# Optimization experiments

Hardware: AMD Instinct MI355X
Metric: run time of the kernel (lower is better)

Reference implementation:

```python
import jax, jax.numpy as jnp
import numpy as np

B, L, EMB, H, NL, E, MAXA, PAD = 64, 512, 400, 256, 3, 512, 32, 0


def setup_inputs() -> dict:
    key = jax.random.key(0)
    ks = jax.random.split(key, 12)
    s = lambda k, shape: jax.random.normal(k, shape, jnp.float32) * 0.02
    Semb = jax.random.normal(ks[0], (B, EMB, L), jnp.float32)
    word_ids = jax.random.randint(ks[1], (B, L), 0, 30000)
    y1 = jax.random.randint(ks[2], (B,), 0, L - MAXA)
    span = jax.random.randint(ks[3], (B,), 0, MAXA)
    y2 = y1 + span
    edges = jax.random.randint(ks[4], (B, E, 2), 0, L)
    return dict(
        Semb=Semb,
        ans_sent_word_ids=word_ids,
        y1_in_sent=y1,
        y2_in_sent=y2,
        edges=edges,
        W1=s(ks[5], (H, EMB)),                 # Initialized_Conv1d (k=1, no bias)
        hw_lin_W=s(ks[6], (2, H, H)), hw_lin_b=jnp.zeros((2, H), jnp.float32),
        hw_gate_W=s(ks[7], (2, H, H)), hw_gate_b=jnp.zeros((2, H), jnp.float32),
        gcn_W=s(ks[8], (NL, H, H)), gcn_b=jnp.zeros((NL, H), jnp.float32),
        conv_W=s(ks[9], (1, NL * H)), conv_b=jnp.zeros((1,), jnp.float32),
        lin_W=s(ks[10], (L, L)), lin_b=jnp.zeros((L,), jnp.float32),
    )


def reference(Semb, ans_sent_word_ids, y1_in_sent, y2_in_sent, edges,
              W1, hw_lin_W, hw_lin_b, hw_gate_W, hw_gate_b,
              gcn_W, gcn_b, conv_W, conv_b, lin_W, lin_b):
    # 1x1 conv: [B, EMB, L] -> [B, H, L]
    x = jnp.einsum('oi,bit->bot', W1, Semb)
    # 2-layer Highway (dropout is identity in eval)
    for i in range(2):
        gate = jax.nn.sigmoid(jnp.einsum('oi,bit->bot', hw_gate_W[i], x) + hw_gate_b[i][None, :, None])
        nonlin = jnp.einsum('oi,bit->bot', hw_lin_W[i], x) + hw_lin_b[i][None, :, None]
        x = gate * nonlin + (1.0 - gate) * x
    maskS = (ans_sent_word_ids != PAD).astype(x.dtype)            # [B, L]
    # answer-span mask (Aemb itself is dead code in the original forward's output)
    pos = y1_in_sent[:, None] + jnp.arange(MAXA)                   # [B, MAXA]
    maskA = (pos <= y2_in_sent[:, None]).astype(x.dtype)
    # dense adjacency from edge list (undirected since gcn_directed=False)
    bidx = jnp.broadcast_to(jnp.arange(B)[:, None], (B, E))
    adj = jnp.zeros((B, L, L), x.dtype)
    adj = adj.at[bidx, edges[..., 0], edges[..., 1]].set(1.0)
    adj = adj.at[bidx, edges[..., 1], edges[..., 0]].set(1.0)
    # GCN (C-GCN style: W(Ax) + W(x), note bias counted twice, /(deg+1), relu)
    h = x.transpose(0, 2, 1)                                       # [B, L, H]
    denom = jnp.sum(adj, axis=2, keepdims=True) + 1.0              # [B, L, 1]
    outs = []
    for l in range(NL):
        Ax = jnp.einsum('bls,bsh->blh', adj, h)
        AxW = jnp.einsum('blh,oh->blo', Ax + h, gcn_W[l]) + 2.0 * gcn_b[l]
        h = jax.nn.relu(AxW / denom)
        outs.append(h)
    cat = jnp.concatenate(outs, axis=2)                            # [B, L, NL*H]
    y = jax.nn.relu(jnp.einsum('blc,oc->bol', cat, conv_W) + conv_b[None, :, None])  # [B,1,L]
    logits = (jnp.einsum('bol,ml->bom', y, lin_W) + lin_b).squeeze(1)                # [B,L]
    logits = logits * maskS + (1.0 - maskS) * (-1e30)
    return (logits, maskA)
```

## Files before the change

### kernel.cpp

```cpp
#include <hip/hip_runtime.h>
#include <cstdint>

#define B 64
#define L 512
#define EMB 400
#define KPAD 416
#define H 256
#define NL 3
#define NE 512
#define MAXA 32
#define M_TOT (B * L)

typedef unsigned short u16;
typedef float f32x4 __attribute__((ext_vector_type(4)));
typedef short short8 __attribute__((ext_vector_type(8)));
typedef u16 u16x8 __attribute__((ext_vector_type(8)));

__device__ __forceinline__ float b2f(u16 u) {
  unsigned v = ((unsigned)u) << 16;
  return __builtin_bit_cast(float, v);
}
__device__ __forceinline__ u16 f2b(float f) {
  unsigned u = __builtin_bit_cast(unsigned, f);
  unsigned r = (u + 0x7fffu + ((u >> 16) & 1u)) >> 16;
  return (u16)r;
}

#define GL16(g, l)                                                              \
  __builtin_amdgcn_global_load_lds((const __attribute__((address_space(1))) void*)(g), \
                                   (__attribute__((address_space(3))) void*)(l), 16, 0, 0)

__global__ __launch_bounds__(256, 2) void k_convT(const float* __restrict__ Semb,
                                                  const u16* __restrict__ W1b,
                                                  u16* __restrict__ Out) {
  __shared__ u16 smem[64 * KPAD + 256 * 32];
  u16* At = smem;
  u16* Bt = smem + 64 * KPAD;
  u16 (*tmp)[72] = (u16(*)[72])Bt;

  const int t = threadIdx.x;
  const int wid = t >> 6, lane = t & 63;
  const int m0 = blockIdx.x * 64;
  const int b = m0 >> 9, l0 = m0 & 511;
  const int fr = lane & 15, kg = lane >> 4;
  const int r4 = t >> 2, ksg = t & 3;

  for (int et = 0; et < 7; ++et) {
    const int e0 = et * 64;
    const int erows = (et < 6) ? 64 : 32;
    {
      const int er = t >> 2, ls = (t & 3) * 16;
      if (er < erows) {
        if (e0 + er < EMB) {
          const float* src = Semb + ((size_t)b * EMB + e0 + er) * L + l0 + ls;
#pragma unroll
          for (int i = 0; i < 4; ++i) {
            const float4 v = *(const float4*)(src + i * 4);
            tmp[er][ls + i * 4 + 0] = f2b(v.x);
            tmp[er][ls + i * 4 + 1] = f2b(v.y);
            tmp[er][ls + i * 4 + 2] = f2b(v.z);
            tmp[er][ls + i * 4 + 3] = f2b(v.w);
          }
        } else {
#pragma unroll
          for (int i = 0; i < 16; ++i) tmp[er][ls + i] = 0;
        }
      }
    }
    __syncthreads();
    {
      const int lr = t >> 2, es = (t & 3) * 16;
      if (es < erows) {
        u16x8 v0, v1;
#pragma unroll
        for (int i = 0; i < 8; ++i) v0[i] = tmp[es + i][lr];
#pragma unroll
        for (int i = 0; i < 8; ++i) v1[i] = tmp[es + 8 + i][lr];
        const int k = e0 + es;
        u16* dst = At + (((size_t)(k >> 5) * 64 + lr) * 4 + ((k & 31) >> 3)) * 8;
        *(u16x8*)dst = v0;
        *(u16x8*)(dst + 8) = v1;
      }
    }
    __syncthreads();
  }

  f32x4 acc[4][4] = {};
  for (int kk = 0; kk < (KPAD >> 5); ++kk) {
    const int kc = kk * 32 + ksg * 8;
#pragma unroll
    for (int c = 0; c < 4; ++c)
      GL16(W1b + (size_t)(c * 64 + r4) * KPAD + kc, Bt + (size_t)(c * 256 + wid * 64) * 8);
    asm volatile("s_waitcnt vmcnt(0)" ::: "memory");
    __builtin_amdgcn_s_barrier();
    asm volatile("" ::: "memory");
    short8 af[4], bf[4];
#pragma unroll
    for (int i = 0; i < 4; ++i) {
      af[i] = *(const short8*)(At + ((size_t)(kk * 64 + i * 16 + fr) * 4 + kg) * 8);
      bf[i] = *(const short8*)(Bt + ((size_t)(wid * 64 + i * 16 + fr) * 4 + kg) * 8);
    }
#pragma unroll
    for (int mi = 0; mi < 4; ++mi)
#pragma unroll
      for (int ni = 0; ni < 4; ++ni)
        acc[mi][ni] = __builtin_amdgcn_mfma_f32_16x16x32_bf16(af[mi], bf[ni], acc[mi][ni], 0, 0, 0);
    __builtin_amdgcn_s_barrier();
    asm volatile("" ::: "memory");
  }

  const int r0 = kg * 4;
  const int c0 = wid * 64 + fr;
#pragma unroll
  for (int ni = 0; ni < 4; ++ni) {
    const int col = c0 + ni * 16;
#pragma unroll
    for (int mi = 0; mi < 4; ++mi)
#pragma unroll
      for (int rr = 0; rr < 4; ++rr)
        Out[(size_t)(m0 + mi * 16 + r0 + rr) * H + col] = f2b(acc[mi][ni][rr]);
  }
}

__global__ __launch_bounds__(256, 2) void gemm64hw(
    const u16* __restrict__ A, const u16* __restrict__ Bw, const u16* __restrict__ B2w,
    const float* __restrict__ bias1, const float* __restrict__ bias2,
    u16* __restrict__ Out) {
  __shared__ u16 Bl[2 * 256 * 32];
  __shared__ u16 Cl[2 * 256 * 32];
  __shared__ u16 Al[2 * 64 * 32];

  const int t = threadIdx.x;
  const int wid = t >> 6, lane = t & 63;
  const int m0 = blockIdx.x * 64;
  const int fr = lane & 15, kg = lane >> 4;
  const int r4 = t >> 2, ksg = t & 3;

  f32x4 acc[4][4] = {};
  f32x4 acc2[4][4] = {};

  for (int kk = 0; kk < 4; ++kk) {
#pragma unroll
    for (int h = 0; h < 2; ++h) {
      const int kc = kk * 64 + h * 32 + ksg * 8;
#pragma unroll
      for (int c = 0; c < 4; ++c) {
        GL16(Bw + (size_t)(c * 64 + r4) * H + kc,
             Bl + (size_t)h * 8192 + (size_t)(c * 256 + wid * 64) * 8);
        GL16(B2w + (size_t)(c * 64 + r4) * H + kc,
             Cl + (size_t)h * 8192 + (size_t)(c * 256 + wid * 64) * 8);
      }
      GL16(A + (size_t)(m0 + r4) * H + kc,
           Al + (size_t)h * 2048 + (size_t)(wid * 64) * 8);
    }
    asm volatile("s_waitcnt vmcnt(0)" ::: "memory");
    __builtin_amdgcn_s_barrier();
    asm volatile("" ::: "memory");
#pragma unroll
    for (int h = 0; h < 2; ++h) {
      short8 af[4], bf[4], cf[4];
#pragma unroll
      for (int i = 0; i < 4; ++i) {
        af[i] = *(const short8*)(Al + (size_t)h * 2048 + ((size_t)(i * 16 + fr) * 4 + kg) * 8);
        bf[i] = *(const short8*)(Bl + (size_t)h * 8192 +
                                 ((size_t)(wid * 64 + i * 16 + fr) * 4 + kg) * 8);
        cf[i] = *(const short8*)(Cl + (size_t)h * 8192 +
                                 ((size_t)(wid * 64 + i * 16 + fr) * 4 + kg) * 8);
      }
#pragma unroll
      for (int mi = 0; mi < 4; ++mi)
#pragma unroll
        for (int ni = 0; ni < 4; ++ni) {
          acc[mi][ni] =
              __builtin_amdgcn_mfma_f32_16x16x32_bf16(af[mi], bf[ni], acc[mi][ni], 0, 0, 0);
          acc2[mi][ni] =
              __builtin_amdgcn_mfma_f32_16x16x32_bf16(af[mi], cf[ni], acc2[mi][ni], 0, 0, 0);
        }
    }
    __builtin_amdgcn_s_barrier();
    asm volatile("" ::: "memory");
  }

  const int r0 = kg * 4;
  const int c0 = wid * 64 + fr;
#pragma unroll
  for (int ni = 0; ni < 4; ++ni) {
    const int col = c0 + ni * 16;
    const float b1 = bias1[col], b2 = bias2[col];
#pragma unroll
    for (int mi = 0; mi < 4; ++mi)
#pragma unroll
      for (int rr = 0; rr < 4; ++rr) {
        const int row = m0 + mi * 16 + r0 + rr;
        const float g = 1.f / (1.f + __expf(-(acc[mi][ni][rr] + b1)));
        const float nn = acc2[mi][ni][rr] + b2;
        const float x = b2f(A[(size_t)row * H + col]);
        Out[(size_t)row * H + col] = f2b(g * nn + (1.f - g) * x);
      }
  }
}

template <bool LAST>
__global__ __launch_bounds__(256, 2) void gemm64gcn(
    const u16* __restrict__ A, const u16* __restrict__ Bw,
    const float* __restrict__ bias1, const float* __restrict__ rden,
    const float* __restrict__ cw, float* __restrict__ yv, u16* __restrict__ Out) {
  __shared__ u16 Bl0[2 * 256 * 32];
  __shared__ u16 Bl1[2 * 256 * 32];
  __shared__ u16 Al0[2 * 64 * 32];
  __shared__ u16 Al1[2 * 64 * 32];

  const int t = threadIdx.x;
  const int wid = t >> 6, lane = t & 63;
  const int m0 = blockIdx.x * 64;
  const int fr = lane & 15, kg = lane >> 4;
  const int r4 = t >> 2, ksg = t & 3;

  f32x4 acc[4][4] = {};

  auto stage = [&](u16* Ab, u16* Bb, int kk) {
#pragma unroll
    for (int h = 0; h < 2; ++h) {
      const int kc = kk * 64 + h * 32 + ksg * 8;
#pragma unroll
      for (int c = 0; c < 4; ++c)
        GL16(Bw + (size_t)(c * 64 + r4) * H + kc,
             Bb + (size_t)h * 8192 + (size_t)(c * 256 + wid * 64) * 8);
      GL16(A + (size_t)(m0 + r4) * H + kc,
           Ab + (size_t)h * 2048 + (size_t)(wid * 64) * 8);
    }
  };
  auto compute = [&](const u16* Ab, const u16* Bb) {
#pragma unroll
    for (int h = 0; h < 2; ++h) {
      short8 af[4], bf[4];
#pragma unroll
      for (int i = 0; i < 4; ++i) {
        af[i] = *(const short8*)(Ab + (size_t)h * 2048 + ((size_t)(i * 16 + fr) * 4 + kg) * 8);
        bf[i] = *(const short8*)(Bb + (size_t)h * 8192 +
                                 ((size_t)(wid * 64 + i * 16 + fr) * 4 + kg) * 8);
      }
#pragma unroll
      for (int mi = 0; mi < 4; ++mi)
#pragma unroll
        for (int ni = 0; ni < 4; ++ni)
          acc[mi][ni] =
              __builtin_amdgcn_mfma_f32_16x16x32_bf16(af[mi], bf[ni], acc[mi][ni], 0, 0, 0);
    }
  };

  const int nk = H >> 6;
  stage(Al0, Bl0, 0);
  for (int kk = 0; kk < nk; ++kk) {
    u16* Ac = (kk & 1) ? Al1 : Al0;
    u16* Bc = (kk & 1) ? Bl1 : Bl0;
    u16* An = (kk & 1) ? Al0 : Al1;
    u16* Bn = (kk & 1) ? Bl0 : Bl1;
    if (kk + 1 < nk) {
      stage(An, Bn, kk + 1);
      asm volatile("s_waitcnt vmcnt(10)" ::: "memory");
    } else {
      asm volatile("s_waitcnt vmcnt(0)" ::: "memory");
    }
    __builtin_amdgcn_s_barrier();
    asm volatile("" ::: "memory");
    compute(Ac, Bc);
    __builtin_amdgcn_s_barrier();
    asm volatile("" ::: "memory");
  }

  const int r0 = kg * 4;
  const int c0 = wid * 64 + fr;
  float ypart[16];
#pragma unroll
  for (int q = 0; q < 16; ++q) ypart[q] = 0.f;
#pragma unroll
  for (int ni = 0; ni < 4; ++ni) {
    const int col = c0 + ni * 16;
    const float b1 = 2.f * bias1[col];
    const float cwv = cw[col];
#pragma unroll
    for (int mi = 0; mi < 4; ++mi)
#pragma unroll
      for (int rr = 0; rr < 4; ++rr) {
        const int row = m0 + mi * 16 + r0 + rr;
        const float s = (acc[mi][ni][rr] + b1) * rden[row];
        const float rl = s > 0.f ? s : 0.f;
        ypart[mi * 4 + rr] += rl * cwv;
        if constexpr (!LAST) Out[(size_t)row * H + col] = f2b(rl);
      }
  }
#pragma unroll
  for (int q = 0; q < 16; ++q) {
    float p = ypart[q];
    p += __shfl_xor(p, 1);
    p += __shfl_xor(p, 2);
    p += __shfl_xor(p, 4);
    p += __shfl_xor(p, 8);
    if (fr == 0) atomicAdd(&yv[m0 + (q >> 2) * 16 + r0 + (q & 3)], p);
  }
}

__global__ __launch_bounds__(256) void k_gather(const unsigned* __restrict__ bm,
                                                const u16* __restrict__ h,
                                                u16* __restrict__ T) {
  const int t = threadIdx.x;
  const int tok = blockIdx.x * 8 + (t >> 5);
  const int b = tok >> 9;
  const int c = (t & 31) * 8;
  const uint4* wp4 = (const uint4*)(bm + (size_t)tok * 16);
  const uint4 w0 = wp4[0], w1 = wp4[1], w2 = wp4[2], w3 = wp4[3];
  const unsigned wa[16] = {w0.x, w0.y, w0.z, w0.w, w1.x, w1.y, w1.z, w1.w,
                           w2.x, w2.y, w2.z, w2.w, w3.x, w3.y, w3.z, w3.w};
  float acc[8];
  {
    const u16x8 v = *(const u16x8*)(h + (size_t)tok * H + c);
#pragma unroll
    for (int i = 0; i < 8; ++i) acc[i] = b2f(v[i]);
  }
#pragma unroll
  for (int wi = 0; wi < 16; ++wi) {
    unsigned bits = wa[wi];
    while (bits) {
      const int bit = __ffs(bits) - 1;
      bits &= bits - 1;
      const int s = wi * 32 + bit;
      const u16x8 u = *(const u16x8*)(h + (size_t)(b * L + s) * H + c);
#pragma unroll
      for (int i = 0; i < 8; ++i) acc[i] += b2f(u[i]);
    }
  }
  u16x8 o;
#pragma unroll
  for (int i = 0; i < 8; ++i) o[i] = f2b(acc[i]);
  *(u16x8*)(T + (size_t)tok * H + c) = o;
}

__global__ __launch_bounds__(256) void k_prep2(const int* __restrict__ edges,
                                               unsigned* __restrict__ bm,
                                               float* __restrict__ rden,
                                               float* __restrict__ yv,
                                               const float* __restrict__ W1,
                                               const float* __restrict__ gW,
                                               const float* __restrict__ lW,
                                               const float* __restrict__ gcnW,
                                               u16* __restrict__ W1b, u16* __restrict__ HWGb,
                                               u16* __restrict__ HWLb, u16* __restrict__ GCNb) {
  const int t = threadIdx.x;
  if (blockIdx.x < B) {
    __shared__ unsigned lbm[512 * 16];
    const int b = blockIdx.x;
#pragma unroll
    for (int i = 0; i < 32; ++i) lbm[i * 256 + t] = 0;
    __syncthreads();
#pragma unroll
    for (int e = 0; e < 2; ++e) {
      const int idx = t * 2 + e;
      const int u = edges[((size_t)b * NE + idx) * 2 + 0];
      const int v = edges[((size_t)b * NE + idx) * 2 + 1];
      atomicOr(&lbm[u * 16 + (v >> 5)], 1u << (v & 31));
      atomicOr(&lbm[v * 16 + (u >> 5)], 1u << (u & 31));
    }
    __syncthreads();
    uint4* gbm = (uint4*)(bm + (size_t)b * 512 * 16);
    const uint4* lb4 = (const uint4*)lbm;
#pragma unroll
    for (int i = 0; i < 8; ++i) gbm[i * 256 + t] = lb4[i * 256 + t];
#pragma unroll
    for (int r = 0; r < 2; ++r) {
      const int row = t * 2 + r;
      int c = 0;
#pragma unroll
      for (int w = 0; w < 16; ++w) c += __popc(lbm[row * 16 + w]);
      rden[(size_t)b * 512 + row] = 1.f / (1.f + (float)c);
    }
#pragma unroll
    for (int i = 0; i < 2; ++i) yv[(size_t)b * 512 + i * 256 + t] = 0.f;
    return;
  }
  int i = (blockIdx.x - B) * 256 + t;
  if (i < 256 * KPAD) {
    const int o = i / KPAD, k = i - o * KPAD;
    W1b[i] = (k < EMB) ? f2b(W1[o * EMB + k]) : (u16)0;
    return;
  }
  i -= 256 * KPAD;
  if (i < 2 * H * H) { HWGb[i] = f2b(gW[i]); return; }
  i -= 2 * H * H;
  if (i < 2 * H * H) { HWLb[i] = f2b(lW[i]); return; }
  i -= 2 * H * H;
  if (i < NL * H * H) GCNb[i] = f2b(gcnW[i]);
}

__global__ __launch_bounds__(256) void k_logits(const float* __restrict__ yv,
                                                const float* __restrict__ cb,
                                                const float* __restrict__ lw,
                                                const float* __restrict__ lb,
                                                const int* __restrict__ wids,
                                                const int* __restrict__ y1,
                                                const int* __restrict__ y2,
                                                float* __restrict__ out) {
  if (blockIdx.x == B * 2) {
#pragma unroll
    for (int j = 0; j < 8; ++j) {
      const int idx = j * 256 + threadIdx.x;
      const int b = idx >> 5, q = idx & 31;
      out[B * L + idx] = (y1[b] + q <= y2[b]) ? 1.0f : 0.0f;
    }
    return;
  }
  const int b = blockIdx.x >> 1;
  const int m = ((blockIdx.x & 1) << 8) + threadIdx.x;
  __shared__ float ys[512];
  const float cb0 = cb[0];
  ys[threadIdx.x] = fmaxf(yv[(size_t)b * L + threadIdx.x] + cb0, 0.f);
  ys[threadIdx.x + 256] = fmaxf(yv[(size_t)b * L + 256 + threadIdx.x] + cb0, 0.f);
  __syncthreads();
  float acc = lb[m];
  const float4* wr = (const float4*)(lw + (size_t)m * L);
#pragma unroll 4
  for (int l4 = 0; l4 < 128; ++l4) {
    const float4 w4 = wr[l4];
    acc += ys[l4 * 4] * w4.x + ys[l4 * 4 + 1] * w4.y + ys[l4 * 4 + 2] * w4.z +
           ys[l4 * 4 + 3] * w4.w;
  }
  out[(size_t)b * L + m] = (wids[(size_t)b * L + m] != 0) ? acc : -1.0e30f;
}

extern "C" void kernel_launch(void* const* d_in, const int* in_sizes, int n_in,
                              void* d_out, int out_size, void* d_ws, size_t ws_size,
                              hipStream_t stream) {
  (void)in_sizes; (void)n_in; (void)out_size; (void)ws_size;
  const float* Semb      = (const float*)d_in[0];
  const int*   wids      = (const int*)d_in[1];
  const int*   y1        = (const int*)d_in[2];
  const int*   y2        = (const int*)d_in[3];
  const int*   edges     = (const int*)d_in[4];
  const float* W1        = (const float*)d_in[5];
  const float* hw_lin_W  = (const float*)d_in[6];
  const float* hw_lin_b  = (const float*)d_in[7];
  const float* hw_gate_W = (const float*)d_in[8];
  const float* hw_gate_b = (const float*)d_in[9];
  const float* gcn_W     = (const float*)d_in[10];
  const float* gcn_b     = (const float*)d_in[11];
  const float* conv_W    = (const float*)d_in[12];
  const float* conv_b    = (const float*)d_in[13];
  const float* lin_W     = (const float*)d_in[14];
  const float* lin_b     = (const float*)d_in[15];
  float* out = (float*)d_out;

  char* ws = (char*)d_ws;
  const size_t SZX = (size_t)M_TOT * H * 2;
  u16* P0b  = (u16*)(ws);
  u16* P1b  = (u16*)(ws + SZX);
  u16* O0   = (u16*)(ws + 2 * SZX);
  u16* O1   = (u16*)(ws + 3 * SZX);
  char* wp  = ws + 4 * SZX;
  u16* W1b  = (u16*)(wp);
  u16* HWGb = (u16*)(wp + 212992);
  u16* HWLb = (u16*)(wp + 212992 + 262144);
  u16* GCNb = (u16*)(wp + 212992 + 2 * 262144);
  char* sp  = wp + 212992 + 2 * 262144 + 393216;
  unsigned* bm   = (unsigned*)(sp);
  float*    yv   = (float*)(sp + 2097152);
  float*    rden = (float*)(sp + 2097152 + 131072);

  const int ncvt = 256 * KPAD + 4 * H * H + NL * H * H;
  k_prep2<<<dim3(B + (ncvt + 255) / 256), 256, 0, stream>>>(
      edges, bm, rden, yv, W1, hw_gate_W, hw_lin_W, gcn_W, W1b, HWGb, HWLb, GCNb);

  k_convT<<<dim3(M_TOT / 64), 256, 0, stream>>>(Semb, W1b, P0b);

  gemm64hw<<<dim3(M_TOT / 64), 256, 0, stream>>>(P0b, HWGb, HWLb, hw_gate_b, hw_lin_b, P1b);
  gemm64hw<<<dim3(M_TOT / 64), 256, 0, stream>>>(P1b, HWGb + H * H, HWLb + H * H,
                                                 hw_gate_b + H, hw_lin_b + H, P0b);

  k_gather<<<dim3(M_TOT / 8), 256, 0, stream>>>(bm, P0b, P1b);
  gemm64gcn<false><<<dim3(M_TOT / 64), 256, 0, stream>>>(P1b, GCNb, gcn_b, rden,
                                                         conv_W, yv, O0);
  k_gather<<<dim3(M_TOT / 8), 256, 0, stream>>>(bm, O0, P0b);
  gemm64gcn<false><<<dim3(M_TOT / 64), 256, 0, stream>>>(P0b, GCNb + H * H, gcn_b + H, rden,
                                                         conv_W + H, yv, O1);
  k_gather<<<dim3(M_TOT / 8), 256, 0, stream>>>(bm, O1, P1b);
  gemm64gcn<true><<<dim3(M_TOT / 64), 256, 0, stream>>>(P1b, GCNb + 2 * H * H, gcn_b + 2 * H,
                                                        rden, conv_W + 2 * H, yv, nullptr);

  k_logits<<<dim3(B * 2 + 1), 256, 0, stream>>>(yv, conv_b, lin_W, lin_b, wids, y1, y2, out);
}
```

Before: 183.2 us.

## Double-buffer highway GEMM LDS staging and read gate weights from global

The highway GEMM now double-buffers the A and first-weight tiles in LDS. The next k-slice is issued before computing the current one, and a partial vmcnt wait lets those loads overlap the MFMA work. The second weight matrix is no longer staged through LDS; each wave reads its fragments straight from global memory, relying on cache hits, which halves LDS staging traffic but puts global-load latency inside the compute loop. The transpose scratch row stride in the conv kernel changes from 72 to 69 elements to alter the LDS bank mapping. An odd stride can break alignment for any wide accesses to that buffer.

```diff
diff --git a/kernel.cpp b/kernel.cpp
--- a/kernel.cpp
+++ b/kernel.cpp
@@ -36,7 +36,7 @@
   __shared__ u16 smem[64 * KPAD + 256 * 32];
   u16* At = smem;
   u16* Bt = smem + 64 * KPAD;
-  u16 (*tmp)[72] = (u16(*)[72])Bt;
+  u16 (*tmp)[69] = (u16(*)[69])Bt;
 
   const int t = threadIdx.x;
   const int wid = t >> 6, lane = t & 63;
@@ -126,9 +126,10 @@
     const u16* __restrict__ A, const u16* __restrict__ Bw, const u16* __restrict__ B2w,
     const float* __restrict__ bias1, const float* __restrict__ bias2,
     u16* __restrict__ Out) {
-  __shared__ u16 Bl[2 * 256 * 32];
-  __shared__ u16 Cl[2 * 256 * 32];
-  __shared__ u16 Al[2 * 64 * 32];
+  __shared__ u16 Bl0[2 * 256 * 32];
+  __shared__ u16 Bl1[2 * 256 * 32];
+  __shared__ u16 Al0[2 * 64 * 32];
+  __shared__ u16 Al1[2 * 64 * 32];
 
   const int t = threadIdx.x;
   const int wid = t >> 6, lane = t & 63;
@@ -139,32 +140,30 @@
   f32x4 acc[4][4] = {};
   f32x4 acc2[4][4] = {};
 
-  for (int kk = 0; kk < 4; ++kk) {
+  auto stage = [&](u16* Ab, u16* Bb, int kk) {
 #pragma unroll
     for (int h = 0; h < 2; ++h) {
       const int kc = kk * 64 + h * 32 + ksg * 8;
 #pragma unroll
-      for (int c = 0; c < 4; ++c) {
+      for (int c = 0; c < 4; ++c)
         GL16(Bw + (size_t)(c * 64 + r4) * H + kc,
-             Bl + (size_t)h * 8192 + (size_t)(c * 256 + wid * 64) * 8);
-        GL16(B2w + (size_t)(c * 64 + r4) * H + kc,
-             Cl + (size_t)h * 8192 + (size_t)(c * 256 + wid * 64) * 8);
-      }
+             Bb + (size_t)h * 8192 + (size_t)(c * 256 + wid * 64) * 8);
       GL16(A + (size_t)(m0 + r4) * H + kc,
-           Al + (size_t)h * 2048 + (size_t)(wid * 64) * 8);
-    }
-    asm volatile("s_waitcnt vmcnt(0)" ::: "memory");
-    __builtin_amdgcn_s_barrier();
-    asm volatile("" ::: "memory");
+           Ab + (size_t)h * 2048 + (size_t)(wid * 64) * 8);
+    }
+  };
+  auto compute = [&](const u16* Ab, const u16* Bb, int kk) {
 #pragma unroll
     for (int h = 0; h < 2; ++h) {
       short8 af[4], bf[4], cf[4];
 #pragma unroll
+      for (int i = 0; i < 4; ++i)
+        cf[i] = *(const short8*)(B2w + (size_t)(wid * 64 + i * 16 + fr) * H +
+                                 kk * 64 + h * 32 + kg * 8);
+#pragma unroll
       for (int i = 0; i < 4; ++i) {
-        af[i] = *(const short8*)(Al + (size_t)h * 2048 + ((size_t)(i * 16 + fr) * 4 + kg) * 8);
-        bf[i] = *(const short8*)(Bl + (size_t)h * 8192 +
-                                 ((size_t)(wid * 64 + i * 16 + fr) * 4 + kg) * 8);
-        cf[i] = *(const short8*)(Cl + (size_t)h * 8192 +
+        af[i] = *(const short8*)(Ab + (size_t)h * 2048 + ((size_t)(i * 16 + fr) * 4 + kg) * 8);
+        bf[i] = *(const short8*)(Bb + (size_t)h * 8192 +
                                  ((size_t)(wid * 64 + i * 16 + fr) * 4 + kg) * 8);
       }
 #pragma unroll
@@ -177,6 +176,24 @@
               __builtin_amdgcn_mfma_f32_16x16x32_bf16(af[mi], cf[ni], acc2[mi][ni], 0, 0, 0);
         }
     }
+  };
+
+  const int nk = H >> 6;
+  stage(Al0, Bl0, 0);
+  for (int kk = 0; kk < nk; ++kk) {
+    u16* Ac = (kk & 1) ? Al1 : Al0;
+    u16* Bc = (kk & 1) ? Bl1 : Bl0;
+    u16* An = (kk & 1) ? Al0 : Al1;
+    u16* Bn = (kk & 1) ? Bl0 : Bl1;
+    if (kk + 1 < nk) {
+      stage(An, Bn, kk + 1);
+      asm volatile("s_waitcnt vmcnt(10)" ::: "memory");
+    } else {
+      asm volatile("s_waitcnt vmcnt(0)" ::: "memory");
+    }
+    __builtin_amdgcn_s_barrier();
+    asm volatile("" ::: "memory");
+    compute(Ac, Bc, kk);
     __builtin_amdgcn_s_barrier();
     asm volatile("" ::: "memory");
   }
```

After: 170.1 us. 1.08x faster.
